# Performance work log

Measured on AMD Instinct MI355X. Metric: run time of the kernel, lower is better.

Reference implementation:

```python
import jax, jax.numpy as jnp
import numpy as np

DIM = 1024
HEADS = 16
HD = DIM // HEADS  # 64
EPS = 1.1920928955078125e-07  # torch.finfo(float32).eps, RMSNorm default


def setup_inputs() -> dict:
    key = jax.random.key(0)
    ks = jax.random.split(key, 8)
    s = 0.02
    return {
        "x": jax.random.normal(ks[0], (2, 2048, DIM), jnp.float32),
        "pe": jax.random.normal(ks[1], (1, 1, 2048, HD // 2, 2, 2), jnp.float32),
        "qkv_w": jax.random.normal(ks[2], (3 * DIM, DIM), jnp.float32) * s,
        "qkv_b": jax.random.normal(ks[3], (3 * DIM,), jnp.float32) * s,
        "q_norm_w": jnp.ones((HD,), jnp.float32),
        "k_norm_w": jnp.ones((HD,), jnp.float32),
        "proj_w": jax.random.normal(ks[4], (DIM, DIM), jnp.float32) * s,
        "proj_b": jax.random.normal(ks[5], (DIM,), jnp.float32) * s,
    }


def _rms_norm(t, w):
    var = jnp.mean(jnp.square(t), axis=-1, keepdims=True)
    return t * jax.lax.rsqrt(var + EPS) * w


def _apply_rope(t, pe):
    # t: [B,H,L,D]; pe: [1,1,L,D/2,2,2]
    B, H, L, D = t.shape
    tp = t.reshape(B, H, L, D // 2, 1, 2)
    out = pe[..., 0] * tp[..., 0] + pe[..., 1] * tp[..., 1]  # [B,H,L,D/2,2]
    return out.reshape(B, H, L, D)


def reference(x, pe, qkv_w, qkv_b, q_norm_w, k_norm_w, proj_w, proj_b):
    B, L, _ = x.shape
    qkv = x @ qkv_w.T + qkv_b  # [B,L,3*DIM]
    qkv = qkv.reshape(B, L, 3, HEADS, HD).transpose(2, 0, 3, 1, 4)  # [3,B,H,L,D]
    q, k, v = qkv[0], qkv[1], qkv[2]
    q = _rms_norm(q, q_norm_w)
    k = _rms_norm(k, k_norm_w)
    q = _apply_rope(q, pe)
    k = _apply_rope(k, pe)
    scale = 1.0 / np.sqrt(HD).astype(np.float32)
    scores = jnp.einsum("bhqd,bhkd->bhqk", q, k) * scale  # [B,H,L,L]
    attn = jax.nn.softmax(scores, axis=-1)
    o = jnp.einsum("bhqk,bhkd->bhqd", attn, v)  # [B,H,L,D]
    o = o.transpose(0, 2, 1, 3).reshape(B, L, DIM)  # B L (H D)
    return o @ proj_w.T + proj_b
```

## Files before the change

### kernel.cpp

```cpp
#include <hip/hip_runtime.h>
#include <hip/hip_bf16.h>

#define DIM   1024
#define HEADS 16
#define HD    64
#define BB    2
#define LL    2048
#define MTOT  (BB*LL)
#define EPSV  1.1920928955078125e-07f

typedef __attribute__((ext_vector_type(8))) short bf16x8;
typedef __attribute__((ext_vector_type(4))) float f32x4;
typedef unsigned short ushort_t;

__device__ __forceinline__ float bf2f(ushort_t u) {
    unsigned int x = ((unsigned int)u) << 16;
    return __builtin_bit_cast(float, x);
}
__device__ __forceinline__ ushort_t f2bf(float f) {
    unsigned int x = __builtin_bit_cast(unsigned int, f);
    unsigned int r = (x + 0x7FFFu + ((x >> 16) & 1u)) >> 16;
    return (ushort_t)r;
}

__global__ __launch_bounds__(256) void f32_to_bf16_k(const float* __restrict__ in,
                                                     ushort_t* __restrict__ out, int n) {
    int i = (blockIdx.x * 256 + threadIdx.x) * 4;
    if (i < n) {
        float4 v = *(const float4*)(in + i);
        ushort4 o;
        o.x = f2bf(v.x); o.y = f2bf(v.y); o.z = f2bf(v.z); o.w = f2bf(v.w);
        *(ushort4*)(out + i) = o;
    }
}

template <int OUT_BF16>
__global__ __launch_bounds__(256) void gemm_bt(const ushort_t* __restrict__ A,
                                               const ushort_t* __restrict__ Bt,
                                               const float* __restrict__ bias,
                                               void* __restrict__ Cout,
                                               int M, int N, int K) {
    __shared__ __attribute__((aligned(16))) ushort_t Asm[128 * 32];
    __shared__ __attribute__((aligned(16))) ushort_t Bsm[128 * 32];
    int tid = threadIdx.x;
    int lane = tid & 63, wid = tid >> 6;
    int wm = wid >> 1, wn = wid & 1;
    int r = lane & 15, g = lane >> 4;
    int m0 = blockIdx.y * 128, n0 = blockIdx.x * 128;

    f32x4 acc[4][4] = {};

    int niter = K >> 5;
    for (int kk = 0; kk < niter; ++kk) {
        int k0 = kk << 5;
        __syncthreads();
#pragma unroll
        for (int p = 0; p < 2; ++p) {
            int off = (p * 256 + tid) * 8;
            int row = off >> 5, col = off & 31;
            int ldsoff = (p * 256 + wid * 64) * 8;
            __builtin_amdgcn_global_load_lds(
                (const __attribute__((address_space(1))) void*)(A + (size_t)(m0 + row) * K + k0 + col),
                (__attribute__((address_space(3))) void*)(Asm + ldsoff), 16, 0, 0);
            __builtin_amdgcn_global_load_lds(
                (const __attribute__((address_space(1))) void*)(Bt + (size_t)(n0 + row) * K + k0 + col),
                (__attribute__((address_space(3))) void*)(Bsm + ldsoff), 16, 0, 0);
        }
        __syncthreads();
        bf16x8 af[4], bfr[4];
#pragma unroll
        for (int mi = 0; mi < 4; mi++)
            af[mi] = *(const bf16x8*)(Asm + (wm * 64 + mi * 16 + r) * 32 + g * 8);
#pragma unroll
        for (int ni = 0; ni < 4; ni++)
            bfr[ni] = *(const bf16x8*)(Bsm + (wn * 64 + ni * 16 + r) * 32 + g * 8);
#pragma unroll
        for (int mi = 0; mi < 4; mi++)
#pragma unroll
            for (int ni = 0; ni < 4; ni++)
                acc[mi][ni] = __builtin_amdgcn_mfma_f32_16x16x32_bf16(af[mi], bfr[ni], acc[mi][ni], 0, 0, 0);
    }
#pragma unroll
    for (int mi = 0; mi < 4; mi++)
#pragma unroll
        for (int ni = 0; ni < 4; ni++) {
            int col = n0 + wn * 64 + ni * 16 + r;
            float bv = bias[col];
#pragma unroll
            for (int reg = 0; reg < 4; reg++) {
                int row = m0 + wm * 64 + mi * 16 + g * 4 + reg;
                float v = acc[mi][ni][reg] + bv;
                if (OUT_BF16)
                    ((ushort_t*)Cout)[(size_t)row * N + col] = f2bf(v);
                else
                    ((float*)Cout)[(size_t)row * N + col] = v;
            }
        }
}

__global__ __launch_bounds__(256) void norm_rope_k(const ushort_t* __restrict__ qkv,
                                                   const float* __restrict__ pe,
                                                   const float* __restrict__ qnw,
                                                   const float* __restrict__ knw,
                                                   ushort_t* __restrict__ qh,
                                                   ushort_t* __restrict__ kh,
                                                   ushort_t* __restrict__ vT) {
    int gtid = blockIdx.x * 256 + threadIdx.x;
    int d = gtid & 63;
    int vid = gtid >> 6;
    int h = vid & 15;
    int t = (vid >> 4) % 3;
    int m = vid / 48;
    int b = m >> 11, l = m & 2047;

    float val = bf2f(qkv[(size_t)m * 3072 + t * 1024 + h * 64 + d]);

    if (t == 2) {
        vT[((size_t)(b * 16 + h) * 64 + d) * 2048 + l] = f2bf(val);
        return;
    }
    float ss = val * val;
#pragma unroll
    for (int off = 1; off < 64; off <<= 1) ss += __shfl_xor(ss, off, 64);
    float rms = rsqrtf(ss * (1.0f / 64.0f) + EPSV);
    const float* nw = (t == 0) ? qnw : knw;
    float nv = val * rms * nw[d];
    float partner = __shfl_xor(nv, 1, 64);
    int j = d & 1;
    float2 pv = *(const float2*)(pe + (size_t)l * 128 + 2 * d);
    float e0 = (j == 0) ? nv : partner;
    float e1 = (j == 0) ? partner : nv;
    float outv = pv.x * e0 + pv.y * e1;
    if (t == 0) outv *= 0.125f;
    ushort_t* dst = (t == 0) ? qh : kh;
    dst[((size_t)(b * 16 + h) * 2048 + l) * 64 + d] = f2bf(outv);
}

__global__ __launch_bounds__(256, 2) void attn_k(const ushort_t* __restrict__ qh,
                                                 const ushort_t* __restrict__ kh,
                                                 const ushort_t* __restrict__ vT,
                                                 ushort_t* __restrict__ ob) {
    __shared__ __attribute__((aligned(16))) ushort_t Ksm[2][64 * 64];
    __shared__ __attribute__((aligned(16))) ushort_t Vsm[2][64 * 64];
    __shared__ __attribute__((aligned(16))) ushort_t Plds[4][2][16 * 64];

    const int tid = threadIdx.x;
    const int lane = tid & 63, wid = tid >> 6;
    const int r = lane & 15, g = lane >> 4;
    const int qt = blockIdx.x, bh = blockIdx.y;
    const int q0 = qt * 128 + wid * 32;
    const ushort_t* Q  = qh + (size_t)bh * LL * 64;
    const ushort_t* Kb = kh + (size_t)bh * LL * 64;
    const ushort_t* Vt = vT + (size_t)bh * 64 * LL;

    int row_[2], ccx_[2];
#pragma unroll
    for (int q = 0; q < 2; ++q) {
        int c = q * 256 + tid;
        row_[q] = c >> 3;
        ccx_[q] = (c & 7) ^ (row_[q] & 7);
    }
    const int swz = (r & 7) * 8;

    bf16x8 qf[2][2];
#pragma unroll
    for (int mf = 0; mf < 2; ++mf)
#pragma unroll
        for (int hf = 0; hf < 2; ++hf)
            qf[mf][hf] = *(const bf16x8*)(Q + (size_t)(q0 + mf * 16 + r) * 64 + hf * 32 + g * 8);

    f32x4 acc[2][4] = {};
    float mrow[2] = {-1e30f, -1e30f};
    float srow[2] = {0.f, 0.f};
    const f32x4 zero = {};

#pragma unroll
    for (int q = 0; q < 2; ++q) {
        __builtin_amdgcn_global_load_lds(
            (const __attribute__((address_space(1))) void*)(Kb + (size_t)row_[q] * 64 + ccx_[q] * 8),
            (__attribute__((address_space(3))) void*)(&Ksm[0][0] + (q * 256 + wid * 64) * 8), 16, 0, 0);
        __builtin_amdgcn_global_load_lds(
            (const __attribute__((address_space(1))) void*)(Vt + (size_t)row_[q] * 2048 + ccx_[q] * 8),
            (__attribute__((address_space(3))) void*)(&Vsm[0][0] + (q * 256 + wid * 64) * 8), 16, 0, 0);
    }
    __syncthreads();

    int buf = 0;
    for (int it = 0; it < 32; ++it) {
        if (it < 31) {
            int kvn = (it + 1) * 64;
#pragma unroll
            for (int q = 0; q < 2; ++q) {
                __builtin_amdgcn_global_load_lds(
                    (const __attribute__((address_space(1))) void*)(Kb + (size_t)(kvn + row_[q]) * 64 + ccx_[q] * 8),
                    (__attribute__((address_space(3))) void*)(&Ksm[buf ^ 1][0] + (q * 256 + wid * 64) * 8), 16, 0, 0);
                __builtin_amdgcn_global_load_lds(
                    (const __attribute__((address_space(1))) void*)(Vt + (size_t)row_[q] * 2048 + kvn + ccx_[q] * 8),
                    (__attribute__((address_space(3))) void*)(&Vsm[buf ^ 1][0] + (q * 256 + wid * 64) * 8), 16, 0, 0);
            }
        }
        const ushort_t* Kl = &Ksm[buf][0];
        const ushort_t* Vl = &Vsm[buf][0];

        bf16x8 kf[4][2];
#pragma unroll
        for (int kt = 0; kt < 4; ++kt)
#pragma unroll
            for (int hf = 0; hf < 2; ++hf)
                kf[kt][hf] = *(const bf16x8*)(Kl + (kt * 16 + r) * 64 + (((hf * 4 + g) * 8) ^ swz));

        f32x4 s[2][4];
        __builtin_amdgcn_s_setprio(1);
#pragma unroll
        for (int mf = 0; mf < 2; ++mf)
#pragma unroll
            for (int kt = 0; kt < 4; ++kt) {
                f32x4 t0 = __builtin_amdgcn_mfma_f32_16x16x32_bf16(kf[kt][0], qf[mf][0], zero, 0, 0, 0);
                s[mf][kt] = __builtin_amdgcn_mfma_f32_16x16x32_bf16(kf[kt][1], qf[mf][1], t0, 0, 0, 0);
            }
        __builtin_amdgcn_s_setprio(0);

#pragma unroll
        for (int mf = 0; mf < 2; ++mf) {
            float pm = -1e30f;
#pragma unroll
            for (int kt = 0; kt < 4; ++kt)
#pragma unroll
                for (int reg = 0; reg < 4; ++reg) pm = fmaxf(pm, s[mf][kt][reg]);
            pm = fmaxf(pm, __shfl_xor(pm, 16, 64));
            pm = fmaxf(pm, __shfl_xor(pm, 32, 64));
            float mn = fmaxf(mrow[mf], pm);
            float al = __expf(mrow[mf] - mn);
            mrow[mf] = mn;
            float rs = 0.f;
#pragma unroll
            for (int kt = 0; kt < 4; ++kt)
#pragma unroll
                for (int reg = 0; reg < 4; ++reg) {
                    float p = __expf(s[mf][kt][reg] - mn);
                    s[mf][kt][reg] = p;
                    rs += p;
                }
            rs += __shfl_xor(rs, 16, 64);
            rs += __shfl_xor(rs, 32, 64);
            srow[mf] = srow[mf] * al + rs;
            float ab[4];
#pragma unroll
            for (int reg = 0; reg < 4; ++reg) ab[reg] = __shfl(al, g * 4 + reg, 16);
#pragma unroll
            for (int dt = 0; dt < 4; ++dt)
#pragma unroll
                for (int reg = 0; reg < 4; ++reg) acc[mf][dt][reg] *= ab[reg];
#pragma unroll
            for (int kt = 0; kt < 4; ++kt) {
                ushort4 pw;
                pw.x = f2bf(s[mf][kt][0]); pw.y = f2bf(s[mf][kt][1]);
                pw.z = f2bf(s[mf][kt][2]); pw.w = f2bf(s[mf][kt][3]);
                *(ushort4*)(&Plds[wid][mf][0] + r * 64 + (((2 * kt + (g >> 1)) * 8) ^ swz) + (g & 1) * 4) = pw;
            }
        }
        asm volatile("s_waitcnt lgkmcnt(0)" ::: "memory");
        __builtin_amdgcn_sched_barrier(0);

        bf16x8 pa[2][2];
#pragma unroll
        for (int mf = 0; mf < 2; ++mf)
#pragma unroll
            for (int hf = 0; hf < 2; ++hf)
                pa[mf][hf] = *(const bf16x8*)(&Plds[wid][mf][0] + r * 64 + (((hf * 4 + g) * 8) ^ swz));

        __builtin_amdgcn_s_setprio(1);
#pragma unroll
        for (int dt = 0; dt < 4; ++dt)
#pragma unroll
            for (int hv = 0; hv < 2; ++hv) {
                bf16x8 vf = *(const bf16x8*)(Vl + (dt * 16 + r) * 64 + (((hv * 4 + g) * 8) ^ swz));
#pragma unroll
                for (int mf = 0; mf < 2; ++mf)
                    acc[mf][dt] = __builtin_amdgcn_mfma_f32_16x16x32_bf16(pa[mf][hv], vf, acc[mf][dt], 0, 0, 0);
            }
        __builtin_amdgcn_s_setprio(0);

        __syncthreads();
        buf ^= 1;
    }

    int b = bh >> 4, h = bh & 15;
#pragma unroll
    for (int mf = 0; mf < 2; ++mf) {
        float sinv = 1.0f / srow[mf];
        float sb[4];
#pragma unroll
        for (int reg = 0; reg < 4; ++reg) sb[reg] = __shfl(sinv, g * 4 + reg, 16);
#pragma unroll
        for (int dt = 0; dt < 4; ++dt)
#pragma unroll
            for (int reg = 0; reg < 4; ++reg) {
                int l = q0 + mf * 16 + g * 4 + reg;
                ob[((size_t)(b * 2048 + l)) * 1024 + h * 64 + dt * 16 + r] =
                    f2bf(acc[mf][dt][reg] * sb[reg]);
            }
    }
}

extern "C" void kernel_launch(void* const* d_in, const int* in_sizes, int n_in,
                              void* d_out, int out_size, void* d_ws, size_t ws_size,
                              hipStream_t stream) {
    const float* x      = (const float*)d_in[0];
    const float* pe     = (const float*)d_in[1];
    const float* qkv_w  = (const float*)d_in[2];
    const float* qkv_b  = (const float*)d_in[3];
    const float* qnw    = (const float*)d_in[4];
    const float* knw    = (const float*)d_in[5];
    const float* proj_w = (const float*)d_in[6];
    const float* proj_b = (const float*)d_in[7];
    float* out = (float*)d_out;

    char* ws = (char*)d_ws;
    ushort_t* xb    = (ushort_t*)(ws);
    ushort_t* wqkv  = (ushort_t*)(ws + 8388608);
    ushort_t* wproj = (ushort_t*)(ws + 8388608 + 6291456);
    ushort_t* qkvb  = (ushort_t*)(ws + 16777216);
    ushort_t* qhp   = (ushort_t*)(ws + 16777216 + 25165824);
    ushort_t* khp   = (ushort_t*)(ws + 16777216 + 25165824 + 8388608);
    ushort_t* vtp   = (ushort_t*)(ws + 16777216 + 25165824 + 2 * 8388608);
    ushort_t* obp   = qkvb;

    f32_to_bf16_k<<<MTOT * DIM / 1024, 256, 0, stream>>>(x, xb, MTOT * DIM);
    f32_to_bf16_k<<<3 * DIM * DIM / 1024, 256, 0, stream>>>(qkv_w, wqkv, 3 * DIM * DIM);
    f32_to_bf16_k<<<DIM * DIM / 1024, 256, 0, stream>>>(proj_w, wproj, DIM * DIM);

    gemm_bt<1><<<dim3(3 * DIM / 128, MTOT / 128), 256, 0, stream>>>(xb, wqkv, qkv_b, qkvb,
                                                                    MTOT, 3 * DIM, DIM);
    norm_rope_k<<<MTOT * 3 * HEADS / 4, 256, 0, stream>>>(qkvb, pe, qnw, knw, qhp, khp, vtp);
    attn_k<<<dim3(16, 32), 256, 0, stream>>>(qhp, khp, vtp, obp);
    gemm_bt<0><<<dim3(DIM / 128, MTOT / 128), 256, 0, stream>>>(obp, wproj, proj_b, out,
                                                                MTOT, DIM, DIM);
}
```

Measured before the change: 260.1 us.

## Vectorize norm/rope with LDS-transposed V writes and lazy softmax rescale

Rewrites the norm+rope kernel so each thread handles four elements with vectorized loads and stores. The V transpose goes through a shared-memory tile, which replaces scattered 2-byte strided writes with coalesced ones. The attention kernel also skips the running-max update and accumulator rescale when every lane's new block max is within 8 of the current max. This removes exps and multiplies but lets unnormalized values grow by up to e^8 in fp32 and bf16 P.

Result: faster. 232.7 us (-10.5%).

```diff
diff --git a/kernel.cpp b/kernel.cpp
--- a/kernel.cpp
+++ b/kernel.cpp
@@ -105,35 +105,67 @@
                                                    ushort_t* __restrict__ qh,
                                                    ushort_t* __restrict__ kh,
                                                    ushort_t* __restrict__ vT) {
-    int gtid = blockIdx.x * 256 + threadIdx.x;
-    int d = gtid & 63;
-    int vid = gtid >> 6;
-    int h = vid & 15;
-    int t = (vid >> 4) % 3;
-    int m = vid / 48;
-    int b = m >> 11, l = m & 2047;
-
-    float val = bf2f(qkv[(size_t)m * 3072 + t * 1024 + h * 64 + d]);
+    __shared__ ushort_t T[64][68];
+    const int tid = threadIdx.x;
+    const int lane = tid & 63, w = tid >> 6;
+    const int rg = lane >> 4;
+    const int d4 = (lane & 15) * 4;
+    const int l0 = blockIdx.x * 64;
+    const int t  = blockIdx.y;
+    const int bh = blockIdx.z;
+    const int b = bh >> 4, h = bh & 15;
 
     if (t == 2) {
-        vT[((size_t)(b * 16 + h) * 64 + d) * 2048 + l] = f2bf(val);
+#pragma unroll
+        for (int i = 0; i < 4; ++i) {
+            int ll = w * 16 + rg + 4 * i;
+            int m = b * 2048 + l0 + ll;
+            ushort4 v = *(const ushort4*)(qkv + (size_t)m * 3072 + 2048 + h * 64 + d4);
+            *(ushort4*)(&T[ll][d4]) = v;
+        }
+        __syncthreads();
+        const int d = tid >> 2, lq = (tid & 3) * 16;
+        ushort_t* dst = vT + ((size_t)(bh * 64 + d)) * 2048 + l0 + lq;
+#pragma unroll
+        for (int c = 0; c < 4; ++c) {
+            ushort4 o;
+            o.x = T[lq + c * 4 + 0][d];
+            o.y = T[lq + c * 4 + 1][d];
+            o.z = T[lq + c * 4 + 2][d];
+            o.w = T[lq + c * 4 + 3][d];
+            *(ushort4*)(dst + c * 4) = o;
+        }
         return;
     }
-    float ss = val * val;
-#pragma unroll
-    for (int off = 1; off < 64; off <<= 1) ss += __shfl_xor(ss, off, 64);
-    float rms = rsqrtf(ss * (1.0f / 64.0f) + EPSV);
-    const float* nw = (t == 0) ? qnw : knw;
-    float nv = val * rms * nw[d];
-    float partner = __shfl_xor(nv, 1, 64);
-    int j = d & 1;
-    float2 pv = *(const float2*)(pe + (size_t)l * 128 + 2 * d);
-    float e0 = (j == 0) ? nv : partner;
-    float e1 = (j == 0) ? partner : nv;
-    float outv = pv.x * e0 + pv.y * e1;
-    if (t == 0) outv *= 0.125f;
+
+    const float* nwp = (t == 0) ? qnw : knw;
+    const float4 nwv = *(const float4*)(nwp + d4);
     ushort_t* dst = (t == 0) ? qh : kh;
-    dst[((size_t)(b * 16 + h) * 2048 + l) * 64 + d] = f2bf(outv);
+    const float qscale = (t == 0) ? 0.125f : 1.0f;
+#pragma unroll
+    for (int i = 0; i < 4; ++i) {
+        int ll = w * 16 + rg + 4 * i;
+        int l = l0 + ll;
+        int m = b * 2048 + l;
+        ushort4 vv = *(const ushort4*)(qkv + (size_t)m * 3072 + t * 1024 + h * 64 + d4);
+        float v0 = bf2f(vv.x), v1 = bf2f(vv.y), v2 = bf2f(vv.z), v3 = bf2f(vv.w);
+        float ss = v0 * v0 + v1 * v1 + v2 * v2 + v3 * v3;
+        ss += __shfl_xor(ss, 1, 64);
+        ss += __shfl_xor(ss, 2, 64);
+        ss += __shfl_xor(ss, 4, 64);
+        ss += __shfl_xor(ss, 8, 64);
+        float rms = rsqrtf(ss * (1.0f / 64.0f) + EPSV);
+        v0 *= rms * nwv.x; v1 *= rms * nwv.y; v2 *= rms * nwv.z; v3 *= rms * nwv.w;
+        float4 p0 = *(const float4*)(pe + (size_t)l * 128 + 2 * d4);
+        float4 p1 = *(const float4*)(pe + (size_t)l * 128 + 2 * d4 + 4);
+        float o0 = (p0.x * v0 + p0.y * v1) * qscale;
+        float o1 = (p0.z * v0 + p0.w * v1) * qscale;
+        float o2 = (p1.x * v2 + p1.y * v3) * qscale;
+        float o3 = (p1.z * v2 + p1.w * v3) * qscale;
+        ushort4 o;
+        o.x = f2bf(o0); o.y = f2bf(o1); o.z = f2bf(o2); o.w = f2bf(o3);
+        *(ushort4*)(dst + ((size_t)bh * 2048 + l) * 64 + d4) = o;
+    }
 }
 
 __global__ __launch_bounds__(256, 2) void attn_k(const ushort_t* __restrict__ qh,
@@ -229,9 +261,15 @@
                 for (int reg = 0; reg < 4; ++reg) pm = fmaxf(pm, s[mf][kt][reg]);
             pm = fmaxf(pm, __shfl_xor(pm, 16, 64));
             pm = fmaxf(pm, __shfl_xor(pm, 32, 64));
-            float mn = fmaxf(mrow[mf], pm);
-            float al = __expf(mrow[mf] - mn);
-            mrow[mf] = mn;
+            bool skip = (__all(pm <= mrow[mf] + 8.0f) != 0);
+            float mn, al;
+            if (skip) {
+                mn = mrow[mf];
+            } else {
+                mn = fmaxf(mrow[mf], pm);
+                al = __expf(mrow[mf] - mn);
+                mrow[mf] = mn;
+            }
             float rs = 0.f;
 #pragma unroll
             for (int kt = 0; kt < 4; ++kt)
@@ -243,14 +281,18 @@
                 }
             rs += __shfl_xor(rs, 16, 64);
             rs += __shfl_xor(rs, 32, 64);
-            srow[mf] = srow[mf] * al + rs;
-            float ab[4];
-#pragma unroll
-            for (int reg = 0; reg < 4; ++reg) ab[reg] = __shfl(al, g * 4 + reg, 16);
-#pragma unroll
-            for (int dt = 0; dt < 4; ++dt)
-#pragma unroll
-                for (int reg = 0; reg < 4; ++reg) acc[mf][dt][reg] *= ab[reg];
+            if (skip) {
+                srow[mf] += rs;
+            } else {
+                srow[mf] = srow[mf] * al + rs;
+                float ab[4];
+#pragma unroll
+                for (int reg = 0; reg < 4; ++reg) ab[reg] = __shfl(al, g * 4 + reg, 16);
+#pragma unroll
+                for (int dt = 0; dt < 4; ++dt)
+#pragma unroll
+                    for (int reg = 0; reg < 4; ++reg) acc[mf][dt][reg] *= ab[reg];
+            }
 #pragma unroll
             for (int kt = 0; kt < 4; ++kt) {
                 ushort4 pw;
@@ -332,7 +374,7 @@
 
     gemm_bt<1><<<dim3(3 * DIM / 128, MTOT / 128), 256, 0, stream>>>(xb, wqkv, qkv_b, qkvb,
                                                                     MTOT, 3 * DIM, DIM);
-    norm_rope_k<<<MTOT * 3 * HEADS / 4, 256, 0, stream>>>(qkvb, pe, qnw, knw, qhp, khp, vtp);
+    norm_rope_k<<<dim3(32, 3, 32), 256, 0, stream>>>(qkvb, pe, qnw, knw, qhp, khp, vtp);
     attn_k<<<dim3(16, 32), 256, 0, stream>>>(qhp, khp, vtp, obp);
     gemm_bt<0><<<dim3(DIM / 128, MTOT / 128), 256, 0, stream>>>(obp, wproj, proj_b, out,
                                                                 MTOT, DIM, DIM);
```
